# Kernel tuning notes

Hardware: AMD Instinct MI355X
Metric: run time of the kernel (lower is better)

## Reference

```python
import jax, jax.numpy as jnp
import numpy as np

B, T, V, H, F = 128, 20, 10000, 512, 49


def _uniform(key, shape, fan):
    s = 1.0 / np.sqrt(fan)
    return jax.random.uniform(key, shape, jnp.float32, -s, s)


def setup_inputs() -> dict:
    key = jax.random.key(0)
    ks = jax.random.split(key, 16)
    return {
        "caption_inputs": jax.random.randint(ks[0], (B, T), 0, V),
        "global_features": jax.random.normal(ks[1], (B, H), jnp.float32),
        "area_features": jax.random.normal(ks[2], (B, H, F), jnp.float32),
        "h0": jnp.zeros((B, H), jnp.float32),
        "c0": jnp.zeros((B, H), jnp.float32),
        # learned params
        "embedding": jax.random.normal(ks[3], (V, H), jnp.float32),
        "W_ih": _uniform(ks[4], (2 * H, 4 * H), H),   # LSTMCell input weights (x @ W_ih)
        "W_hh": _uniform(ks[5], (H, 4 * H), H),
        "b_ih": _uniform(ks[6], (4 * H,), H),
        "b_hh": _uniform(ks[7], (4 * H,), H),
        "Wv": _uniform(ks[8], (H, H), H),             # attention comp_visual
        "Wh": _uniform(ks[9], (H, H), H),             # attention comp_hidden
        "wo": _uniform(ks[10], (H,), H),              # attention output_layer
        "W_out": _uniform(ks[11], (2 * H, V), 2 * H), # decoder output layer
        "b_out": _uniform(ks[12], (V,), 2 * H),
    }


def reference(caption_inputs, global_features, area_features, h0, c0,
              embedding, W_ih, W_hh, b_ih, b_hh, Wv, Wh, wo, W_out, b_out):
    # Precompute attention visual projection (time-invariant): [B,F,H]
    feat = jnp.swapaxes(area_features, 1, 2)          # [B,F,H]
    Vproj = jnp.einsum('bfh,hk->bfk', feat, Wv)       # [B,F,H]
    bias = b_ih + b_hh

    def step(carry, tok):
        h, c = carry
        emb = embedding[tok]                           # [B,H]
        x = jnp.concatenate([emb, global_features], axis=1)   # [B,2H]
        gates = x @ W_ih + h @ W_hh + bias             # [B,4H]
        i, f, g, o = jnp.split(gates, 4, axis=1)
        c = jax.nn.sigmoid(f) * c + jax.nn.sigmoid(i) * jnp.tanh(g)
        h = jax.nn.sigmoid(o) * jnp.tanh(c)
        # spatial attention over F locations
        z = jnp.tanh(Vproj + (h @ Wh)[:, None, :])     # [B,F,H]
        scores = jnp.einsum('bfh,h->bf', z, wo)        # [B,F]
        alpha = jax.nn.softmax(scores, axis=1)
        attended = jnp.einsum('bhf,bf->bh', area_features, alpha)  # [B,H]
        out = jnp.concatenate([h, attended], axis=1) @ W_out + b_out  # [B,V]
        return (h, c), out

    (_, _), outs = jax.lax.scan(step, (h0, c0), caption_inputs.T)  # [T,B,V]
    return jnp.swapaxes(outs, 0, 1)                    # [B,T,V]
```

## Files before the change

### kernel.cpp

```cpp
#include <hip/hip_runtime.h>

#define B_ 128
#define T_ 20
#define V_ 10000
#define H_ 512
#define F_ 49
#define NBLK_ 128

typedef unsigned short u16;
typedef __attribute__((ext_vector_type(8))) short short8;
typedef __attribute__((ext_vector_type(4))) float floatx4;
typedef __attribute__((ext_vector_type(2))) float floatx2;

#define GLOBAL_AS __attribute__((address_space(1)))
#define LDS_AS    __attribute__((address_space(3)))

__device__ inline void load_lds16(const void* g, void* l) {
    __builtin_amdgcn_global_load_lds((const GLOBAL_AS void*)g, (LDS_AS void*)l, 16, 0, 0);
}

__device__ inline u16 f2b(float v) {
    unsigned u = __builtin_bit_cast(unsigned, v);
    unsigned rounding = 0x7FFFu + ((u >> 16) & 1u);
    return (u16)((u + rounding) >> 16);
}
__device__ inline float b2f(u16 h) {
    unsigned u = ((unsigned)h) << 16;
    return __builtin_bit_cast(float, u);
}
__device__ inline float fast_tanh(float x) {
    return 1.f - 2.f / (__expf(2.f * x) + 1.f);
}
__device__ inline float sigm(float x) { return 1.f / (1.f + __expf(-x)); }

__device__ __forceinline__ void tr32(const float* __restrict__ src, u16* __restrict__ dst,
                                     int K, int N, int bx, int by, int tx, int ty,
                                     float (*tl)[33]) {
    int n0 = bx * 32, k0 = by * 32;
    #pragma unroll
    for (int i = 0; i < 32; i += 8) {
        int k = k0 + ty + i, n = n0 + tx;
        tl[ty + i][tx] = (k < K && n < N) ? src[(size_t)k * N + n] : 0.f;
    }
    __syncthreads();
    #pragma unroll
    for (int i = 0; i < 32; i += 8) {
        int n = n0 + ty + i, k = k0 + tx;
        if (n < N && k < K) dst[(size_t)n * K + k] = f2b(tl[tx][ty + i]);
    }
}

__global__ __launch_bounds__(256) void preamble(
        const float* __restrict__ W_ih, const float* __restrict__ W_hh,
        const float* __restrict__ Wv, const float* __restrict__ Wh,
        const float* __restrict__ W_out, const int* __restrict__ cap,
        const float* __restrict__ emb, const float* __restrict__ gf,
        const float* __restrict__ area, const float* __restrict__ h0,
        u16* __restrict__ WihT, u16* __restrict__ WhhT, u16* __restrict__ WvT,
        u16* __restrict__ WhT, u16* __restrict__ WoutT, u16* __restrict__ X,
        u16* __restrict__ feat, u16* __restrict__ Hall, int* __restrict__ bar) {
    __shared__ float tl[32][33];
    const int bid = blockIdx.x, tid = threadIdx.x;
    const int tx = tid & 31, ty = tid >> 5;

    if (bid < 2048) {
        int r = bid;                 tr32(W_ih, WihT, 1024, 2048, r % 64, r / 64, tx, ty, tl);
    } else if (bid < 3072) {
        int r = bid - 2048;          tr32(W_hh, WhhT, 512, 2048, r % 64, r / 64, tx, ty, tl);
    } else if (bid < 3328) {
        int r = bid - 3072;          tr32(Wv, WvT, 512, 512, r % 16, r / 16, tx, ty, tl);
    } else if (bid < 3584) {
        int r = bid - 3328;          tr32(Wh, WhT, 512, 512, r % 16, r / 16, tx, ty, tl);
    } else if (bid < 13600) {
        int r = bid - 3584;          tr32(W_out, WoutT, 1024, 10000, r % 313, r / 313, tx, ty, tl);
    } else if (bid < 16160) {
        int r = bid - 13600;
        int t = r / B_, b = r % B_;
        int tok = cap[b * T_ + t];
        for (int col = tid; col < 2 * H_; col += 256) {
            float v = (col < H_) ? emb[(size_t)tok * H_ + col] : gf[(size_t)b * H_ + (col - H_)];
            X[(size_t)r * (2 * H_) + col] = f2b(v);
        }
    } else if (bid < 20256) {
        int r = bid - 16160;
        int b = r >> 5, t32 = r & 31;
        int fx = t32 & 1, hy = t32 >> 1;
        tr32(area + (size_t)b * H_ * F_, feat + (size_t)b * F_ * H_,
             H_, F_, fx, hy, tx, ty, tl);
    } else {
        int r = bid - 20256;
        int i = r * 256 + tid;
        Hall[i] = f2b(h0[i]);
        if (r < 8) bar[r * 256 + tid] = 0;
    }
}

__global__ __launch_bounds__(256, 1) void decode_loop(
        const u16* __restrict__ WhhT, const float* __restrict__ Xin,
        const float* __restrict__ c0, u16* __restrict__ Hall,
        int* __restrict__ bar) {

    __shared__ __align__(16) u16 Whs[128 * 512];
    __shared__ __align__(16) u16 hstage[16 * 512];
    __shared__ float gl[4 * 16 * 32];
    __shared__ float csh[16 * 32];

    const int tid = threadIdx.x;
    const int wave = tid >> 6, lane = tid & 63;
    const int lm = lane & 15, q = lane >> 4;
    const int bid = blockIdx.x;
    const int mg = bid & 7, jg = bid >> 3;

    const int row = tid >> 4, jj = (tid & 15) * 2;
    const int grow = mg * 16 + row;
    const int j = jg * 32 + jj;

    #pragma unroll
    for (int i = 0; i < 32; ++i) {
        int r = i * 4 + wave;
        int g = r >> 5, jr = r & 31;
        int wrow = g * H_ + jg * 32 + jr;
        load_lds16(WhhT + (size_t)wrow * H_ + (size_t)(lane ^ (r & 7)) * 8,
                   (char*)Whs + r * 1024);
    }
    csh[row * 32 + jj]     = c0[(size_t)grow * H_ + j];
    csh[row * 32 + jj + 1] = c0[(size_t)grow * H_ + j + 1];

    floatx2 xf[4];
    {
        const float* xb = Xin + (size_t)grow * (4 * H_) + j;
        #pragma unroll
        for (int g = 0; g < 4; ++g) xf[g] = *(const floatx2*)(xb + g * H_);
    }

    for (int t = 0; t < T_; ++t) {
        const u16* hprev = Hall + (size_t)t * B_ * H_;
        u16* hnext = Hall + (size_t)(t + 1) * B_ * H_;

        #pragma unroll
        for (int i = 0; i < 4; ++i) {
            int r = i * 4 + wave;
            load_lds16(hprev + (size_t)(mg * 16 + r) * H_ + (size_t)(lane ^ (r & 7)) * 8,
                       (char*)hstage + r * 1024);
        }
        __syncthreads();

        floatx4 acc0 = {0.f, 0.f, 0.f, 0.f}, acc1 = {0.f, 0.f, 0.f, 0.f};
        #pragma unroll
        for (int kt = 0; kt < 16; ++kt) {
            int ch = kt * 4 + q;
            int sw = (ch ^ (lm & 7)) << 3;
            short8 a  = *(const short8*)&hstage[(lm << 9) + sw];
            short8 b0 = *(const short8*)&Whs[((wave * 32 + lm) << 9) + sw];
            short8 b1 = *(const short8*)&Whs[((wave * 32 + 16 + lm) << 9) + sw];
            acc0 = __builtin_amdgcn_mfma_f32_16x16x32_bf16(a, b0, acc0, 0, 0, 0);
            acc1 = __builtin_amdgcn_mfma_f32_16x16x32_bf16(a, b1, acc1, 0, 0, 0);
        }
        #pragma unroll
        for (int r = 0; r < 4; ++r) {
            gl[wave * 512 + (q * 4 + r) * 32 + lm]      = acc0[r];
            gl[wave * 512 + (q * 4 + r) * 32 + 16 + lm] = acc1[r];
        }
        __syncthreads();

        floatx2 xc[4];
        #pragma unroll
        for (int g = 0; g < 4; ++g) xc[g] = xf[g];
        if (t + 1 < T_) {
            const float* xb = Xin + ((size_t)(t + 1) * B_ + grow) * (4 * H_) + j;
            #pragma unroll
            for (int g = 0; g < 4; ++g) xf[g] = *(const floatx2*)(xb + g * H_);
        }

        {
            float gi0 = gl[0 * 512 + row * 32 + jj]     + xc[0][0];
            float gi1 = gl[0 * 512 + row * 32 + jj + 1] + xc[0][1];
            float gf0 = gl[1 * 512 + row * 32 + jj]     + xc[1][0];
            float gf1 = gl[1 * 512 + row * 32 + jj + 1] + xc[1][1];
            float gg0 = gl[2 * 512 + row * 32 + jj]     + xc[2][0];
            float gg1 = gl[2 * 512 + row * 32 + jj + 1] + xc[2][1];
            float go0 = gl[3 * 512 + row * 32 + jj]     + xc[3][0];
            float go1 = gl[3 * 512 + row * 32 + jj + 1] + xc[3][1];
            float c0n = sigm(gf0) * csh[row * 32 + jj]     + sigm(gi0) * fast_tanh(gg0);
            float c1n = sigm(gf1) * csh[row * 32 + jj + 1] + sigm(gi1) * fast_tanh(gg1);
            csh[row * 32 + jj]     = c0n;
            csh[row * 32 + jj + 1] = c1n;
            unsigned hv = (unsigned)f2b(sigm(go0) * fast_tanh(c0n)) |
                          ((unsigned)f2b(sigm(go1) * fast_tanh(c1n)) << 16);
            *(unsigned*)(hnext + (size_t)grow * H_ + j) = hv;
        }

        if (t + 1 < T_) {
            __syncthreads();
            if (tid == 0)
                __hip_atomic_store(&bar[(mg * 16 + jg) * 16], t + 1,
                                   __ATOMIC_RELEASE, __HIP_MEMORY_SCOPE_AGENT);
            if (wave == 0) {
                int fl = (lane < 16)
                    ? __hip_atomic_load(&bar[(mg * 16 + lane) * 16],
                                        __ATOMIC_RELAXED, __HIP_MEMORY_SCOPE_AGENT)
                    : (t + 1);
                while (__any(fl < t + 1)) {
                    __builtin_amdgcn_s_sleep(1);
                    fl = (lane < 16)
                        ? __hip_atomic_load(&bar[(mg * 16 + lane) * 16],
                                            __ATOMIC_RELAXED, __HIP_MEMORY_SCOPE_AGENT)
                        : (t + 1);
                }
                if (lane == 0)
                    (void)__hip_atomic_load(&bar[(mg * 16) * 16],
                                            __ATOMIC_ACQUIRE, __HIP_MEMORY_SCOPE_AGENT);
            }
            __syncthreads();
        }
    }
}

__global__ __launch_bounds__(256) void attn_post(
        const float* __restrict__ ahbuf, const u16* __restrict__ Vprojb,
        const u16* __restrict__ feat, const float* __restrict__ wo,
        const u16* __restrict__ Hall, u16* __restrict__ Hcat) {
    __shared__ __align__(16) u16 Vsh[F_ * H_];
    __shared__ __align__(16) u16 fsh[F_ * H_];
    __shared__ float ash[H_];
    __shared__ float wosh[H_];
    __shared__ float sc[64];

    const int tid = threadIdx.x;
    const int wave = tid >> 6, lane = tid & 63;
    const int b = blockIdx.x >> 1, th = blockIdx.x & 1;

    const short8* vsrc = (const short8*)(Vprojb + (size_t)b * F_ * H_);
    const short8* fsrc = (const short8*)(feat + (size_t)b * F_ * H_);
    for (int i = tid; i < F_ * H_ / 8; i += 256) {
        ((short8*)Vsh)[i] = vsrc[i];
        ((short8*)fsh)[i] = fsrc[i];
    }
    for (int i = tid; i < H_; i += 256) wosh[i] = wo[i];
    __syncthreads();

    for (int t = th * (T_ / 2); t < (th + 1) * (T_ / 2); ++t) {
        for (int i = tid; i < H_; i += 256)
            ash[i] = ahbuf[((size_t)t * B_ + b) * H_ + i];
        __syncthreads();

        for (int f = wave; f < F_; f += 4) {
            short8 vv = *(const short8*)&Vsh[f * H_ + lane * 8];
            float s = 0.f;
            #pragma unroll
            for (int e = 0; e < 8; ++e) {
                int h = lane * 8 + e;
                s += wosh[h] * fast_tanh(b2f((u16)vv[e]) + ash[h]);
            }
            #pragma unroll
            for (int off = 32; off; off >>= 1) s += __shfl_xor(s, off);
            if (lane == 0) sc[f] = s;
        }
        __syncthreads();

        if (tid < 64) {
            float v = (tid < F_) ? sc[tid] : -1e30f;
            float m = v;
            #pragma unroll
            for (int off = 32; off; off >>= 1) m = fmaxf(m, __shfl_xor(m, off));
            float e = (tid < F_) ? __expf(v - m) : 0.f;
            float sum = e;
            #pragma unroll
            for (int off = 32; off; off >>= 1) sum += __shfl_xor(sum, off);
            if (tid < F_) sc[tid] = e / sum;
        }
        __syncthreads();

        const size_t rowo = ((size_t)b * T_ + t) * (2 * H_);
        const short8* hrow = (const short8*)(Hall + ((size_t)(t + 1) * B_ + b) * H_);
        for (int i = tid; i < H_ / 8; i += 256)
            ((short8*)(Hcat + rowo))[i] = hrow[i];
        for (int h = tid; h < H_; h += 256) {
            float acc = 0.f;
            #pragma unroll
            for (int f = 0; f < F_; ++f) acc += b2f(fsh[f * H_ + h]) * sc[f];
            Hcat[rowo + H_ + h] = f2b(acc);
        }
        __syncthreads();
    }
}

template <int WRITE_BF16>
__device__ __forceinline__ void gemm2_body(
        const u16* __restrict__ A, int lda, const u16* __restrict__ Bt, int ldb,
        void* __restrict__ Cout, int ldc, const float* __restrict__ bias1,
        const float* __restrict__ bias2, int M, int N, int K, int bx, int by,
        u16* As, u16* Bs) {
    const int tid = threadIdx.x, wave = tid >> 6, lane = tid & 63;
    const int wr = wave >> 1, wc = wave & 1;
    const int lm = lane & 15, q = lane >> 4;
    const int m0 = bx * 128, n0 = by * 128;

    const int off = wave * 1024 + lane * 16;
    const int r0 = off >> 6;
    const int c0 = (off & 63) >> 1;

    const u16* gA0 = A + (size_t)(m0 + r0) * lda + c0;
    const u16* gA1 = A + (size_t)(m0 + r0 + 64) * lda + c0;
    int nb0 = n0 + r0;      if (nb0 > N - 1) nb0 = N - 1;
    int nb1 = n0 + r0 + 64; if (nb1 > N - 1) nb1 = N - 1;
    const u16* gB0 = Bt + (size_t)nb0 * ldb + c0;
    const u16* gB1 = Bt + (size_t)nb1 * ldb + c0;

    floatx4 acc[4][4];
    #pragma unroll
    for (int i = 0; i < 4; ++i)
        #pragma unroll
        for (int jq = 0; jq < 4; ++jq) acc[i][jq] = floatx4{0.f, 0.f, 0.f, 0.f};

    const int nkt = K >> 5;
    {
        load_lds16(gA0, (char*)As + wave * 1024);
        load_lds16(gA1, (char*)As + 4096 + wave * 1024);
        load_lds16(gB0, (char*)Bs + wave * 1024);
        load_lds16(gB1, (char*)Bs + 4096 + wave * 1024);
    }
    __syncthreads();

    int cur = 0;
    for (int kt = 0; kt < nkt; ++kt) {
        if (kt + 1 < nkt) {
            const int ko = (kt + 1) * 32;
            char* dA = (char*)(As + (cur ^ 1) * 4096);
            char* dB = (char*)(Bs + (cur ^ 1) * 4096);
            load_lds16(gA0 + ko, dA + wave * 1024);
            load_lds16(gA1 + ko, dA + 4096 + wave * 1024);
            load_lds16(gB0 + ko, dB + wave * 1024);
            load_lds16(gB1 + ko, dB + 4096 + wave * 1024);
        }
        const u16* Ab = As + cur * 4096;
        const u16* Bb = Bs + cur * 4096;
        short8 af[4], bf[4];
        #pragma unroll
        for (int i = 0; i < 4; ++i)
            af[i] = *(const short8*)&Ab[(wr * 64 + i * 16 + lm) * 32 + q * 8];
        #pragma unroll
        for (int jq = 0; jq < 4; ++jq)
            bf[jq] = *(const short8*)&Bb[(wc * 64 + jq * 16 + lm) * 32 + q * 8];
        #pragma unroll
        for (int i = 0; i < 4; ++i)
            #pragma unroll
            for (int jq = 0; jq < 4; ++jq)
                acc[i][jq] = __builtin_amdgcn_mfma_f32_16x16x32_bf16(af[i], bf[jq], acc[i][jq], 0, 0, 0);
        __syncthreads();
        cur ^= 1;
    }

    #pragma unroll
    for (int i = 0; i < 4; ++i) {
        const int row = m0 + wr * 64 + i * 16 + q * 4;
        #pragma unroll
        for (int jq = 0; jq < 4; ++jq) {
            const int col = n0 + wc * 64 + jq * 16 + lm;
            if (col < N) {
                #pragma unroll
                for (int r = 0; r < 4; ++r) {
                    float v = acc[i][jq][r];
                    if (bias1) v += bias1[col];
                    if (bias2) v += bias2[col];
                    if (WRITE_BF16) ((u16*)Cout)[(size_t)(row + r) * ldc + col] = f2b(v);
                    else            ((float*)Cout)[(size_t)(row + r) * ldc + col] = v;
                }
            }
        }
    }
}

template <int WRITE_BF16>
__global__ __launch_bounds__(256) void gemm2(const u16* __restrict__ A, int lda,
                                             const u16* __restrict__ Bt, int ldb,
                                             void* __restrict__ Cout, int ldc,
                                             const float* __restrict__ bias1,
                                             const float* __restrict__ bias2,
                                             int M, int N, int K) {
    __shared__ __align__(16) u16 As[2 * 128 * 32];
    __shared__ __align__(16) u16 Bs[2 * 128 * 32];
    const int nbx = gridDim.x;
    const int nwg = nbx * gridDim.y;
    const int lin = blockIdx.x + blockIdx.y * nbx;
    const int qq = nwg >> 3, rr = nwg & 7;
    const int xcd = lin & 7, idx = lin >> 3;
    const int wg = (xcd < rr ? xcd * (qq + 1) : rr * (qq + 1) + (xcd - rr) * qq) + idx;
    gemm2_body<WRITE_BF16>(A, lda, Bt, ldb, Cout, ldc, bias1, bias2, M, N, K,
                           wg % nbx, wg / nbx, As, Bs);
}

__global__ __launch_bounds__(256) void gemm_pair(
        const u16* __restrict__ X, const u16* __restrict__ WihT,
        float* __restrict__ Xin, const float* __restrict__ b_ih,
        const float* __restrict__ b_hh, const u16* __restrict__ feat,
        const u16* __restrict__ WvT, u16* __restrict__ Vprojb) {
    __shared__ __align__(16) u16 As[2 * 128 * 32];
    __shared__ __align__(16) u16 Bs[2 * 128 * 32];
    int bid = blockIdx.x;
    if (bid < 320) {
        gemm2_body<0>(X, 2 * H_, WihT, 2 * H_, Xin, 4 * H_, b_ih, b_hh,
                      T_ * B_, 4 * H_, 2 * H_, bid % 20, bid / 20, As, Bs);
    } else {
        int r = bid - 320;
        gemm2_body<1>(feat, H_, WvT, H_, Vprojb, H_, nullptr, nullptr,
                      B_ * F_, H_, H_, r % 49, r / 49, As, Bs);
    }
}

extern "C" void kernel_launch(void* const* d_in, const int* in_sizes, int n_in,
                              void* d_out, int out_size, void* d_ws, size_t ws_size,
                              hipStream_t stream) {
    const int*   cap   = (const int*)d_in[0];
    const float* gf    = (const float*)d_in[1];
    const float* area  = (const float*)d_in[2];
    const float* h0    = (const float*)d_in[3];
    const float* c0    = (const float*)d_in[4];
    const float* emb   = (const float*)d_in[5];
    const float* W_ih  = (const float*)d_in[6];
    const float* W_hh  = (const float*)d_in[7];
    const float* b_ih  = (const float*)d_in[8];
    const float* b_hh  = (const float*)d_in[9];
    const float* Wv    = (const float*)d_in[10];
    const float* Wh    = (const float*)d_in[11];
    const float* wo    = (const float*)d_in[12];
    const float* W_out = (const float*)d_in[13];
    const float* b_out = (const float*)d_in[14];
    float* out = (float*)d_out;

    char* p = (char*)d_ws;
    auto alloc = [&](size_t bytes) {
        char* q = p;
        p += (bytes + 255) & ~(size_t)255;
        return q;
    };
    u16*   X      = (u16*)alloc((size_t)T_ * B_ * 2 * H_ * 2);
    u16*   WihT   = (u16*)alloc((size_t)4 * H_ * 2 * H_ * 2);
    u16*   WhhT   = (u16*)alloc((size_t)4 * H_ * H_ * 2);
    u16*   WvT    = (u16*)alloc((size_t)H_ * H_ * 2);
    u16*   WhT    = (u16*)alloc((size_t)H_ * H_ * 2);
    u16*   WoutT  = (u16*)alloc((size_t)V_ * 2 * H_ * 2);
    u16*   feat   = (u16*)alloc((size_t)B_ * F_ * H_ * 2);
    float* Xin    = (float*)alloc((size_t)T_ * B_ * 4 * H_ * 4);
    u16*   Vprojb = (u16*)alloc((size_t)B_ * F_ * H_ * 2);
    float* ahbuf  = (float*)alloc((size_t)T_ * B_ * H_ * 4);
    u16*   Hall   = (u16*)alloc((size_t)(T_ + 1) * B_ * H_ * 2);
    int*   bar    = (int*)alloc(8192);
    u16*   Hcat   = (u16*)alloc((size_t)B_ * T_ * 2 * H_ * 2);

    preamble<<<20512, 256, 0, stream>>>(W_ih, W_hh, Wv, Wh, W_out, cap, emb, gf,
                                        area, h0, WihT, WhhT, WvT, WhT, WoutT,
                                        X, feat, Hall, bar);

    gemm_pair<<<516, 256, 0, stream>>>(X, WihT, Xin, b_ih, b_hh, feat, WvT, Vprojb);

    decode_loop<<<NBLK_, 256, 0, stream>>>(WhhT, Xin, c0, Hall, bar);

    gemm2<0><<<dim3(T_ * B_ / 128, H_ / 128), 256, 0, stream>>>(
        Hall + (size_t)B_ * H_, H_, WhT, H_, ahbuf, H_, nullptr, nullptr, T_ * B_, H_, H_);

    attn_post<<<2 * B_, 256, 0, stream>>>(ahbuf, Vprojb, feat, wo, Hall, Hcat);

    gemm2<0><<<dim3(T_ * B_ / 128, (V_ + 127) / 128), 256, 0, stream>>>(
        Hcat, 2 * H_, WoutT, 2 * H_, out, V_, b_out, nullptr, T_ * B_, V_, 2 * H_);
}
```

Before: 569.2 us.

## Use dedicated 256x256-tile GEMM with XCD-aware swizzle for output projection

Replaces the generic 128x128 GEMM used for the final [2560x1024]x[1024x10000] output projection with a new kernel using 256x256 tiles, 512 threads, and K-step 64. The kernel double-buffers LDS via direct global-to-LDS loads with an XOR swizzle, and remaps workgroups across the 8 XCDs for cache locality. It also raises wave priority around MFMA bursts. The larger tiles cut redundant operand loads, but they cost occupancy (one block per CU), leave only 400 blocks, and add padded work on the last N tile.

```diff
diff --git a/kernel.cpp b/kernel.cpp
--- a/kernel.cpp
+++ b/kernel.cpp
@@ -408,6 +408,111 @@
     }
 }
 
+__global__ __launch_bounds__(512, 1) void gemm_out(
+        const u16* __restrict__ A, int lda, const u16* __restrict__ Bt, int ldb,
+        float* __restrict__ Cout, int ldc, const float* __restrict__ bias1,
+        int M, int N, int K) {
+    __shared__ __align__(16) u16 As[2 * 16384];
+    __shared__ __align__(16) u16 Bs[2 * 16384];
+
+    const int tid = threadIdx.x;
+    const int wave = tid >> 6, lane = tid & 63;
+    const int lm = lane & 15, q = lane >> 4;
+    const int wm = wave >> 2, wn = wave & 3;
+
+    const int nbx = gridDim.x;
+    const int nwg = nbx * gridDim.y;
+    const int lin = blockIdx.x + blockIdx.y * nbx;
+    const int qq = nwg >> 3, rr = nwg & 7;
+    const int xcd = lin & 7, idx = lin >> 3;
+    const int wg = (xcd < rr ? xcd * (qq + 1) : rr * (qq + 1) + (xcd - rr) * qq) + idx;
+    const int m0 = (wg % nbx) * 256, n0 = (wg / nbx) * 256;
+
+    const int r8 = lane >> 3;
+    const int gch = (lane & 7) ^ r8;
+
+    floatx4 acc[8][4];
+    #pragma unroll
+    for (int i = 0; i < 8; ++i)
+        #pragma unroll
+        for (int jn = 0; jn < 4; ++jn) acc[i][jn] = floatx4{0.f, 0.f, 0.f, 0.f};
+
+    const int nkt = K >> 6;
+
+    auto STAGE = [&](int kt2) {
+        u16* Ad = As + (kt2 & 1) * 16384;
+        u16* Bd = Bs + (kt2 & 1) * 16384;
+        const int kb = kt2 * 64;
+        #pragma unroll
+        for (int i = 0; i < 4; ++i) {
+            int rw = i * 8 + wave;
+            int rowA = rw * 8 + r8;
+            load_lds16(A + (size_t)(m0 + rowA) * lda + kb + gch * 8,
+                       (char*)Ad + rw * 1024);
+        }
+        #pragma unroll
+        for (int i = 0; i < 4; ++i) {
+            int rw = i * 8 + wave;
+            int rowB = rw * 8 + r8;
+            int nb = n0 + rowB; if (nb > N - 1) nb = N - 1;
+            load_lds16(Bt + (size_t)nb * ldb + kb + gch * 8,
+                       (char*)Bd + rw * 1024);
+        }
+    };
+
+    STAGE(0);
+    __syncthreads();
+
+    for (int kt = 0; kt < nkt; ++kt) {
+        const u16* Ab = As + (kt & 1) * 16384;
+        const u16* Bb = Bs + (kt & 1) * 16384;
+        if (kt + 1 < nkt) STAGE(kt + 1);
+
+        #pragma unroll
+        for (int kk = 0; kk < 2; ++kk) {
+            const int chs = ((kk * 4 + q) ^ (lm & 7)) * 8;
+            short8 bF[4];
+            #pragma unroll
+            for (int fn = 0; fn < 4; ++fn)
+                bF[fn] = *(const short8*)(Bb + (size_t)(wn * 64 + fn * 16 + lm) * 64 + chs);
+            #pragma unroll
+            for (int mh = 0; mh < 2; ++mh) {
+                short8 aF[4];
+                #pragma unroll
+                for (int f = 0; f < 4; ++f)
+                    aF[f] = *(const short8*)(Ab + (size_t)(wm * 128 + mh * 64 + f * 16 + lm) * 64 + chs);
+                __builtin_amdgcn_s_barrier();
+                __builtin_amdgcn_s_setprio(1);
+                #pragma unroll
+                for (int f = 0; f < 4; ++f)
+                    #pragma unroll
+                    for (int fn = 0; fn < 4; ++fn)
+                        acc[mh * 4 + f][fn] = __builtin_amdgcn_mfma_f32_16x16x32_bf16(
+                            aF[f], bF[fn], acc[mh * 4 + f][fn], 0, 0, 0);
+                __builtin_amdgcn_s_setprio(0);
+                __builtin_amdgcn_s_barrier();
+            }
+        }
+        asm volatile("s_waitcnt vmcnt(0)" ::: "memory");
+        __builtin_amdgcn_s_barrier();
+    }
+
+    #pragma unroll
+    for (int fm = 0; fm < 8; ++fm) {
+        const int row = m0 + wm * 128 + fm * 16 + q * 4;
+        #pragma unroll
+        for (int fn = 0; fn < 4; ++fn) {
+            const int col = n0 + wn * 64 + fn * 16 + lm;
+            if (col < N) {
+                float bv = bias1[col];
+                #pragma unroll
+                for (int r = 0; r < 4; ++r)
+                    Cout[(size_t)(row + r) * ldc + col] = acc[fm][fn][r] + bv;
+            }
+        }
+    }
+}
+
 extern "C" void kernel_launch(void* const* d_in, const int* in_sizes, int n_in,
                               void* d_out, int out_size, void* d_ws, size_t ws_size,
                               hipStream_t stream) {
@@ -461,6 +566,6 @@
 
     attn_post<<<2 * B_, 256, 0, stream>>>(ahbuf, Vprojb, feat, wo, Hall, Hcat);
 
-    gemm2<0><<<dim3(T_ * B_ / 128, (V_ + 127) / 128), 256, 0, stream>>>(
-        Hcat, 2 * H_, WoutT, 2 * H_, out, V_, b_out, nullptr, T_ * B_, V_, 2 * H_);
-}
+    gemm_out<<<dim3(T_ * B_ / 256, (V_ + 255) / 256), 512, 0, stream>>>(
+        Hcat, 2 * H_, WoutT, 2 * H_, out, V_, b_out, T_ * B_, V_, 2 * H_);
+}
```

Result: no change. 561.2 us (-1.4%).
